# Kernel tuning notes

Hardware: AMD Instinct MI355X
Metric: run time of the kernel (lower is better)

## Reference

```python
import jax, jax.numpy as jnp
import numpy as np

N_DEG = 5
RANK = 4
SCALE = 4
IMW = IMH = 512
S = IMW * IMH
BATCH = 64
C_CH = 1


def setup_inputs() -> dict:
    key = jax.random.key(0)
    k1, k2, k3, k4 = jax.random.split(key, 4)
    x = jax.random.normal(k1, (BATCH, C_CH, IMW // SCALE, IMH // SCALE), dtype=jnp.float32)
    # CP-decomposed polynomial (CCP) factors; small init keeps degree-5 products stable
    A = jax.random.normal(k2, (N_DEG, RANK, S), dtype=jnp.float32) * 0.01
    C = jax.random.normal(k3, (S, RANK), dtype=jnp.float32) * 0.01
    b = jax.random.normal(k4, (S,), dtype=jnp.float32) * 0.01
    return {"x": x, "A": A, "C": C, "b": b}


def reference(x, A, C, b):
    bsize, c, w, h = x.shape
    # bilinear upsample, align_corners=False (half-pixel, matches torch default)
    up = jax.image.resize(x, (bsize, c, w * SCALE, h * SCALE), method="bilinear")
    flat = up.reshape(bsize, c, S)
    v = flat[:, c - 1, :]  # [B, S] -- original applies PolyLayer only to channel c-1
    # CCP polynomial network: z1 = A1 v; z_n = (A_n v) * z_{n-1} + z_{n-1}
    za = jnp.einsum("nrs,bs->bnr", A, v)  # [B, N, rank]
    z = za[:, 0]
    for n in range(1, N_DEG):
        z = za[:, n] * z + z
    out_v = jnp.einsum("br,sr->bs", z, C) + b  # [B, S]
    flat = flat.at[:, c - 1, :].set(out_v)
    return flat.reshape(bsize, c, w * SCALE, h * SCALE)
```

## Files before the change

### kernel.cpp

```cpp
#include <hip/hip_runtime.h>

#define S_TOTAL (512 * 512)
#define BATCH 64
#define KTOT2 16384

typedef float vfloat4 __attribute__((ext_vector_type(4)));
typedef float vfloat2 __attribute__((ext_vector_type(2)));

__device__ __forceinline__ float swz_x1(float v) {
    return __int_as_float(__builtin_amdgcn_ds_swizzle(__float_as_int(v), 0x041F));
}
__device__ __forceinline__ float swz_x2(float v) {
    return __int_as_float(__builtin_amdgcn_ds_swizzle(__float_as_int(v), 0x081F));
}
__device__ __forceinline__ float swz_x4(float v) {
    return __int_as_float(__builtin_amdgcn_ds_swizzle(__float_as_int(v), 0x101F));
}
__device__ __forceinline__ float swz_x8(float v) {
    return __int_as_float(__builtin_amdgcn_ds_swizzle(__float_as_int(v), 0x201F));
}

__global__ __launch_bounds__(256) void adjxy_kernel(
    const float* __restrict__ A,
    float* __restrict__ B2)
{
    __shared__ float arows[20][512];
    __shared__ float b1loc[20][128];

    const int t  = threadIdx.x;
    const int nr = blockIdx.x >> 5;
    const int tc = blockIdx.x & 31;
    const int y0 = 16 * tc - 2;

    const float* An = A + (size_t)nr * S_TOTAL;
#pragma unroll
    for (int i = t; i < 20 * 128; i += 256) {
        const int rl = i >> 7;
        const int q  = i & 127;
        const int y  = y0 + rl;
        vfloat4 v = {0.0f, 0.0f, 0.0f, 0.0f};
        if (y >= 0 && y < 512)
            v = *(const vfloat4*)(An + (size_t)y * 512 + q * 4);
        *(vfloat4*)&arows[rl][q * 4] = v;
    }
    __syncthreads();

#pragma unroll
    for (int i = t; i < 20 * 128; i += 256) {
        const int rl = i >> 7;
        const int j  = i & 127;
        const int base = 4 * j;
        const vfloat4 m0 = *(const vfloat4*)&arows[rl][max(base - 4, 0)];
        const vfloat4 m1 = *(const vfloat4*)&arows[rl][base];
        const vfloat4 m2 = *(const vfloat4*)&arows[rl][min(base + 4, 508)];
        float e0 = m0.z, e1 = m0.w, e6 = m2.x, e7 = m2.y;
        if (j == 0)   { e0 = 0.0f; e1 = 0.0f; }
        if (j == 127) { e6 = 0.0f; e7 = 0.0f; }
        float s = 0.125f * e0 + 0.375f * e1
                + 0.625f * m1.x + 0.875f * m1.y
                + 0.875f * m1.z + 0.625f * m1.w
                + 0.375f * e6 + 0.125f * e7;
        if (j == 0)   s += 0.375f * arows[rl][0]   + 0.125f * arows[rl][1];
        if (j == 127) s += 0.125f * arows[rl][510] + 0.375f * arows[rl][511];
        b1loc[rl][j] = s;
    }
    __syncthreads();

    const float w[8] = {0.125f, 0.375f, 0.625f, 0.875f,
                        0.875f, 0.625f, 0.375f, 0.125f};
#pragma unroll
    for (int i = t; i < 512; i += 256) {
        const int tyl = i >> 7;
        const int j   = i & 127;
        const int ty  = tc * 4 + tyl;
        float s = 0.0f;
#pragma unroll
        for (int p = 0; p < 8; ++p)
            s = fmaf(w[p], b1loc[4 * tyl + p][j], s);
        if (ty == 0)   s += 0.375f * b1loc[2][j]  + 0.125f * b1loc[3][j];
        if (ty == 127) s += 0.125f * b1loc[16][j] + 0.375f * b1loc[17][j];
        B2[(size_t)nr * KTOT2 + ty * 128 + j] = s;
    }
}

__global__ __launch_bounds__(512) void za_partial_kernel(
    const float* __restrict__ x,
    const float* __restrict__ B2,
    float* __restrict__ partial)
{
    const int t    = threadIdx.x;
    const int blk  = blockIdx.x;
    const int w    = t >> 6;
    const int lane = t & 63;
    const int b0   = w * 8;
    const size_t kbase = (size_t)blk * 256 + 4 * lane;

    vfloat4 xv[8];
#pragma unroll
    for (int bi = 0; bi < 8; ++bi)
        xv[bi] = *(const vfloat4*)(x + (size_t)(b0 + bi) * KTOT2 + kbase);

    float* pb = partial + (size_t)blk * 1280;
    const int lane1 = lane & 1, lane2 = lane & 2, lane4 = lane & 4, lane8 = lane & 8;

#pragma unroll
    for (int ch = 0; ch < 2; ++ch) {
        float acc[16][5];
#pragma unroll
        for (int v = 0; v < 16; ++v)
#pragma unroll
            for (int tt = 0; tt < 5; ++tt) acc[v][tt] = 0.0f;

#pragma unroll
        for (int tt = 0; tt < 5; ++tt)
#pragma unroll
            for (int par = 0; par < 2; ++par) {
                const int nr = ch * 10 + 2 * tt + par;
                const vfloat4 bq = *(const vfloat4*)(B2 + (size_t)nr * KTOT2 + kbase);
#pragma unroll
                for (int bi = 0; bi < 8; ++bi) {
                    acc[bi * 2 + par][tt] =
                        fmaf(bq.x, xv[bi].x, fmaf(bq.y, xv[bi].y,
                        fmaf(bq.z, xv[bi].z, fmaf(bq.w, xv[bi].w,
                             acc[bi * 2 + par][tt]))));
                }
            }

        float s1[8][5];
#pragma unroll
        for (int v = 0; v < 8; ++v)
#pragma unroll
            for (int tt = 0; tt < 5; ++tt) {
                const float u = acc[v][tt], h = acc[v + 8][tt];
                s1[v][tt] = (lane1 ? h : u) + swz_x1(lane1 ? u : h);
            }
        float s2[4][5];
#pragma unroll
        for (int v = 0; v < 4; ++v)
#pragma unroll
            for (int tt = 0; tt < 5; ++tt) {
                const float u = s1[v][tt], h = s1[v + 4][tt];
                s2[v][tt] = (lane2 ? h : u) + swz_x2(lane2 ? u : h);
            }
        float s3[2][5];
#pragma unroll
        for (int v = 0; v < 2; ++v)
#pragma unroll
            for (int tt = 0; tt < 5; ++tt) {
                const float u = s2[v][tt], h = s2[v + 2][tt];
                s3[v][tt] = (lane4 ? h : u) + swz_x4(lane4 ? u : h);
            }
        float s4[5];
#pragma unroll
        for (int tt = 0; tt < 5; ++tt) {
            const float u = s3[0][tt], h = s3[1][tt];
            s4[tt] = (lane8 ? h : u) + swz_x8(lane8 ? u : h);
        }
#pragma unroll
        for (int tt = 0; tt < 5; ++tt) {
            s4[tt] += __shfl_xor(s4[tt], 16, 64);
            s4[tt] += __shfl_xor(s4[tt], 32, 64);
        }

        if (lane < 16) {
            const int m = ((lane & 1) << 3) | ((lane & 2) << 1) |
                          ((lane & 4) >> 1) | ((lane & 8) >> 3);
            float* dst = pb + (b0 + (m >> 1)) * 20 + ch * 10 + (m & 1);
#pragma unroll
            for (int tt = 0; tt < 5; ++tt) dst[2 * tt] = s4[tt];
        }
    }
}

__global__ __launch_bounds__(256) void za_reduce_kernel(
    const float* __restrict__ partial, float* __restrict__ za)
{
    const int c = blockIdx.x * 256 + threadIdx.x;
    float a0 = 0, a1 = 0, a2 = 0, a3 = 0;
    for (int r = 0; r < 64; r += 4) {
        a0 += partial[(size_t)(r + 0) * 1280 + c];
        a1 += partial[(size_t)(r + 1) * 1280 + c];
        a2 += partial[(size_t)(r + 2) * 1280 + c];
        a3 += partial[(size_t)(r + 3) * 1280 + c];
    }
    za[c] = (a0 + a1) + (a2 + a3);
}

__global__ __launch_bounds__(256) void out_kernel(
    const float* __restrict__ C,
    const float* __restrict__ bias,
    const float* __restrict__ za,
    float* __restrict__ out)
{
    __shared__ float zs[BATCH][4];
    const int t = threadIdx.x;
    if (t < 64) {
#pragma unroll
        for (int r = 0; r < 4; ++r) {
            float zv = za[t * 20 + r];
#pragma unroll
            for (int n = 1; n < 5; ++n)
                zv *= (1.0f + za[t * 20 + n * 4 + r]);
            zs[t][r] = zv;
        }
    }
    __syncthreads();

    const int s0 = (blockIdx.x * 256 + t) * 2;
    const vfloat4 c0 = *(const vfloat4*)(C + (size_t)s0 * 4);
    const vfloat4 c1 = *(const vfloat4*)(C + (size_t)s0 * 4 + 4);
    const vfloat2 bv = *(const vfloat2*)(bias + s0);

#pragma unroll 8
    for (int bb = 0; bb < BATCH; ++bb) {
        const float z0 = zs[bb][0], z1 = zs[bb][1];
        const float z2 = zs[bb][2], z3 = zs[bb][3];
        vfloat2 o;
        o.x = fmaf(z0, c0.x, fmaf(z1, c0.y, fmaf(z2, c0.z, fmaf(z3, c0.w, bv.x))));
        o.y = fmaf(z0, c1.x, fmaf(z1, c1.y, fmaf(z2, c1.z, fmaf(z3, c1.w, bv.y))));
        __builtin_nontemporal_store(o, (vfloat2*)(out + (size_t)bb * S_TOTAL + s0));
    }
}

extern "C" void kernel_launch(void* const* d_in, const int* in_sizes, int n_in,
                              void* d_out, int out_size, void* d_ws, size_t ws_size,
                              hipStream_t stream)
{
    const float* x    = (const float*)d_in[0];
    const float* A    = (const float*)d_in[1];
    const float* C    = (const float*)d_in[2];
    const float* bias = (const float*)d_in[3];
    float* out = (float*)d_out;

    float* B2      = (float*)d_ws;
    float* partial = B2 + (size_t)20 * KTOT2;
    float* za      = partial + (size_t)64 * 1280;

    adjxy_kernel<<<640, 256, 0, stream>>>(A, B2);
    za_partial_kernel<<<64, 512, 0, stream>>>(x, B2, partial);
    za_reduce_kernel<<<5, 256, 0, stream>>>(partial, za);
    out_kernel<<<512, 256, 0, stream>>>(C, bias, za, out);
}
```

Baseline: 35.87 us.

## Fuse za reduction into partial kernel via last-block ticket and drop LDS staging

Removes the separate za_reduce kernel: each za_partial block increments an atomic counter, and the last block to finish sums all partials and computes the per-batch polynomial z values, writing them to a small global buffer. out_kernel now just loads the precomputed z values instead of recomputing them in every block. adjxy_kernel reads A directly from global memory rather than staging rows in shared memory first. A memset is added to reset the counter each call, and the final reduction runs serially in a single block.

```diff
diff --git a/kernel.cpp b/kernel.cpp
--- a/kernel.cpp
+++ b/kernel.cpp
@@ -3,6 +3,7 @@
 #define S_TOTAL (512 * 512)
 #define BATCH 64
 #define KTOT2 16384
+#define NBLK_ZA 64
 
 typedef float vfloat4 __attribute__((ext_vector_type(4)));
 typedef float vfloat2 __attribute__((ext_vector_type(2)));
@@ -24,7 +25,6 @@
     const float* __restrict__ A,
     float* __restrict__ B2)
 {
-    __shared__ float arows[20][512];
     __shared__ float b1loc[20][128];
 
     const int t  = threadIdx.x;
@@ -33,35 +33,29 @@
     const int y0 = 16 * tc - 2;
 
     const float* An = A + (size_t)nr * S_TOTAL;
-#pragma unroll
-    for (int i = t; i < 20 * 128; i += 256) {
-        const int rl = i >> 7;
-        const int q  = i & 127;
-        const int y  = y0 + rl;
-        vfloat4 v = {0.0f, 0.0f, 0.0f, 0.0f};
-        if (y >= 0 && y < 512)
-            v = *(const vfloat4*)(An + (size_t)y * 512 + q * 4);
-        *(vfloat4*)&arows[rl][q * 4] = v;
-    }
-    __syncthreads();
 
 #pragma unroll
     for (int i = t; i < 20 * 128; i += 256) {
         const int rl = i >> 7;
         const int j  = i & 127;
-        const int base = 4 * j;
-        const vfloat4 m0 = *(const vfloat4*)&arows[rl][max(base - 4, 0)];
-        const vfloat4 m1 = *(const vfloat4*)&arows[rl][base];
-        const vfloat4 m2 = *(const vfloat4*)&arows[rl][min(base + 4, 508)];
-        float e0 = m0.z, e1 = m0.w, e6 = m2.x, e7 = m2.y;
-        if (j == 0)   { e0 = 0.0f; e1 = 0.0f; }
-        if (j == 127) { e6 = 0.0f; e7 = 0.0f; }
-        float s = 0.125f * e0 + 0.375f * e1
-                + 0.625f * m1.x + 0.875f * m1.y
-                + 0.875f * m1.z + 0.625f * m1.w
-                + 0.375f * e6 + 0.125f * e7;
-        if (j == 0)   s += 0.375f * arows[rl][0]   + 0.125f * arows[rl][1];
-        if (j == 127) s += 0.125f * arows[rl][510] + 0.375f * arows[rl][511];
+        const int y  = y0 + rl;
+        float s = 0.0f;
+        if (y >= 0 && y < 512) {
+            const float* Ay = An + (size_t)y * 512;
+            const int base = 4 * j;
+            const vfloat4 m0 = *(const vfloat4*)(Ay + max(base - 4, 0));
+            const vfloat4 m1 = *(const vfloat4*)(Ay + base);
+            const vfloat4 m2 = *(const vfloat4*)(Ay + min(base + 4, 508));
+            float e0 = m0.z, e1 = m0.w, e6 = m2.x, e7 = m2.y;
+            if (j == 0)   { e0 = 0.0f; e1 = 0.0f; }
+            if (j == 127) { e6 = 0.0f; e7 = 0.0f; }
+            s = 0.125f * e0 + 0.375f * e1
+              + 0.625f * m1.x + 0.875f * m1.y
+              + 0.875f * m1.z + 0.625f * m1.w
+              + 0.375f * e6 + 0.125f * e7;
+            if (j == 0)   s += 0.375f * Ay[0]   + 0.125f * Ay[1];
+            if (j == 127) s += 0.125f * Ay[510] + 0.375f * Ay[511];
+        }
         b1loc[rl][j] = s;
     }
     __syncthreads();
@@ -86,8 +80,13 @@
 __global__ __launch_bounds__(512) void za_partial_kernel(
     const float* __restrict__ x,
     const float* __restrict__ B2,
-    float* __restrict__ partial)
-{
+    float* __restrict__ partial,
+    float* __restrict__ zg,
+    unsigned int* __restrict__ counter)
+{
+    __shared__ float za_lds[1280];
+    __shared__ unsigned int ticket;
+
     const int t    = threadIdx.x;
     const int blk  = blockIdx.x;
     const int w    = t >> 6;
@@ -170,40 +169,46 @@
             for (int tt = 0; tt < 5; ++tt) dst[2 * tt] = s4[tt];
         }
     }
-}
-
-__global__ __launch_bounds__(256) void za_reduce_kernel(
-    const float* __restrict__ partial, float* __restrict__ za)
-{
-    const int c = blockIdx.x * 256 + threadIdx.x;
-    float a0 = 0, a1 = 0, a2 = 0, a3 = 0;
-    for (int r = 0; r < 64; r += 4) {
-        a0 += partial[(size_t)(r + 0) * 1280 + c];
-        a1 += partial[(size_t)(r + 1) * 1280 + c];
-        a2 += partial[(size_t)(r + 2) * 1280 + c];
-        a3 += partial[(size_t)(r + 3) * 1280 + c];
-    }
-    za[c] = (a0 + a1) + (a2 + a3);
+
+    __threadfence();
+    __syncthreads();
+    if (t == 0) ticket = atomicAdd(counter, 1u);
+    __syncthreads();
+    if (ticket != NBLK_ZA - 1) return;
+
+    __threadfence();
+    for (int c = t; c < 1280; c += 512) {
+        float a0 = 0, a1 = 0, a2 = 0, a3 = 0;
+        for (int r = 0; r < NBLK_ZA; r += 4) {
+            a0 += partial[(size_t)(r + 0) * 1280 + c];
+            a1 += partial[(size_t)(r + 1) * 1280 + c];
+            a2 += partial[(size_t)(r + 2) * 1280 + c];
+            a3 += partial[(size_t)(r + 3) * 1280 + c];
+        }
+        za_lds[c] = (a0 + a1) + (a2 + a3);
+    }
+    __syncthreads();
+    if (t < 64) {
+#pragma unroll
+        for (int r = 0; r < 4; ++r) {
+            float zv = za_lds[t * 20 + r];
+#pragma unroll
+            for (int n = 1; n < 5; ++n)
+                zv *= (1.0f + za_lds[t * 20 + n * 4 + r]);
+            zg[t * 4 + r] = zv;
+        }
+    }
 }
 
 __global__ __launch_bounds__(256) void out_kernel(
     const float* __restrict__ C,
     const float* __restrict__ bias,
-    const float* __restrict__ za,
+    const float* __restrict__ zg,
     float* __restrict__ out)
 {
-    __shared__ float zs[BATCH][4];
+    __shared__ float zs[256];
     const int t = threadIdx.x;
-    if (t < 64) {
-#pragma unroll
-        for (int r = 0; r < 4; ++r) {
-            float zv = za[t * 20 + r];
-#pragma unroll
-            for (int n = 1; n < 5; ++n)
-                zv *= (1.0f + za[t * 20 + n * 4 + r]);
-            zs[t][r] = zv;
-        }
-    }
+    zs[t] = zg[t];
     __syncthreads();
 
     const int s0 = (blockIdx.x * 256 + t) * 2;
@@ -213,8 +218,8 @@
 
 #pragma unroll 8
     for (int bb = 0; bb < BATCH; ++bb) {
-        const float z0 = zs[bb][0], z1 = zs[bb][1];
-        const float z2 = zs[bb][2], z3 = zs[bb][3];
+        const float z0 = zs[bb * 4 + 0], z1 = zs[bb * 4 + 1];
+        const float z2 = zs[bb * 4 + 2], z3 = zs[bb * 4 + 3];
         vfloat2 o;
         o.x = fmaf(z0, c0.x, fmaf(z1, c0.y, fmaf(z2, c0.z, fmaf(z3, c0.w, bv.x))));
         o.y = fmaf(z0, c1.x, fmaf(z1, c1.y, fmaf(z2, c1.z, fmaf(z3, c1.w, bv.y))));
@@ -234,10 +239,11 @@
 
     float* B2      = (float*)d_ws;
     float* partial = B2 + (size_t)20 * KTOT2;
-    float* za      = partial + (size_t)64 * 1280;
-
+    float* zg      = partial + (size_t)NBLK_ZA * 1280;
+    unsigned int* counter = (unsigned int*)(zg + 256);
+
+    hipMemsetAsync(counter, 0, sizeof(unsigned int), stream);
     adjxy_kernel<<<640, 256, 0, stream>>>(A, B2);
-    za_partial_kernel<<<64, 512, 0, stream>>>(x, B2, partial);
-    za_reduce_kernel<<<5, 256, 0, stream>>>(partial, za);
-    out_kernel<<<512, 256, 0, stream>>>(C, bias, za, out);
-}
+    za_partial_kernel<<<NBLK_ZA, 512, 0, stream>>>(x, B2, partial, zg, counter);
+    out_kernel<<<512, 256, 0, stream>>>(C, bias, zg, out);
+}
```

Result: slower. 63.75 us (+77.7%).

## Spread za_partial over more blocks, widen out stores, drop adjxy LDS staging

Applied to the files above, without the earlier changes.

za_partial now launches four blocks per K chunk, each wave handling two batches instead of eight. This quadruples the grid and reduces register pressure and the length of the swizzle reduction. The out kernel writes float4 per thread and splits the batch range between two blocks, giving wider nontemporal stores. adjxy reads A directly from global memory instead of staging rows in LDS, which removes one barrier but issues redundant overlapping global loads.

```diff
diff --git a/kernel.cpp b/kernel.cpp
--- a/kernel.cpp
+++ b/kernel.cpp
@@ -3,9 +3,9 @@
 #define S_TOTAL (512 * 512)
 #define BATCH 64
 #define KTOT2 16384
+#define NKC 64
 
 typedef float vfloat4 __attribute__((ext_vector_type(4)));
-typedef float vfloat2 __attribute__((ext_vector_type(2)));
 
 __device__ __forceinline__ float swz_x1(float v) {
     return __int_as_float(__builtin_amdgcn_ds_swizzle(__float_as_int(v), 0x041F));
@@ -24,7 +24,6 @@
     const float* __restrict__ A,
     float* __restrict__ B2)
 {
-    __shared__ float arows[20][512];
     __shared__ float b1loc[20][128];
 
     const int t  = threadIdx.x;
@@ -33,35 +32,29 @@
     const int y0 = 16 * tc - 2;
 
     const float* An = A + (size_t)nr * S_TOTAL;
-#pragma unroll
-    for (int i = t; i < 20 * 128; i += 256) {
-        const int rl = i >> 7;
-        const int q  = i & 127;
-        const int y  = y0 + rl;
-        vfloat4 v = {0.0f, 0.0f, 0.0f, 0.0f};
-        if (y >= 0 && y < 512)
-            v = *(const vfloat4*)(An + (size_t)y * 512 + q * 4);
-        *(vfloat4*)&arows[rl][q * 4] = v;
-    }
-    __syncthreads();
 
 #pragma unroll
     for (int i = t; i < 20 * 128; i += 256) {
         const int rl = i >> 7;
         const int j  = i & 127;
-        const int base = 4 * j;
-        const vfloat4 m0 = *(const vfloat4*)&arows[rl][max(base - 4, 0)];
-        const vfloat4 m1 = *(const vfloat4*)&arows[rl][base];
-        const vfloat4 m2 = *(const vfloat4*)&arows[rl][min(base + 4, 508)];
-        float e0 = m0.z, e1 = m0.w, e6 = m2.x, e7 = m2.y;
-        if (j == 0)   { e0 = 0.0f; e1 = 0.0f; }
-        if (j == 127) { e6 = 0.0f; e7 = 0.0f; }
-        float s = 0.125f * e0 + 0.375f * e1
-                + 0.625f * m1.x + 0.875f * m1.y
-                + 0.875f * m1.z + 0.625f * m1.w
-                + 0.375f * e6 + 0.125f * e7;
-        if (j == 0)   s += 0.375f * arows[rl][0]   + 0.125f * arows[rl][1];
-        if (j == 127) s += 0.125f * arows[rl][510] + 0.375f * arows[rl][511];
+        const int y  = y0 + rl;
+        float s = 0.0f;
+        if (y >= 0 && y < 512) {
+            const float* Ay = An + (size_t)y * 512;
+            const int base = 4 * j;
+            const vfloat4 m0 = *(const vfloat4*)(Ay + max(base - 4, 0));
+            const vfloat4 m1 = *(const vfloat4*)(Ay + base);
+            const vfloat4 m2 = *(const vfloat4*)(Ay + min(base + 4, 508));
+            float e0 = m0.z, e1 = m0.w, e6 = m2.x, e7 = m2.y;
+            if (j == 0)   { e0 = 0.0f; e1 = 0.0f; }
+            if (j == 127) { e6 = 0.0f; e7 = 0.0f; }
+            s = 0.125f * e0 + 0.375f * e1
+              + 0.625f * m1.x + 0.875f * m1.y
+              + 0.875f * m1.z + 0.625f * m1.w
+              + 0.375f * e6 + 0.125f * e7;
+            if (j == 0)   s += 0.375f * Ay[0]   + 0.125f * Ay[1];
+            if (j == 127) s += 0.125f * Ay[510] + 0.375f * Ay[511];
+        }
         b1loc[rl][j] = s;
     }
     __syncthreads();
@@ -89,25 +82,24 @@
     float* __restrict__ partial)
 {
     const int t    = threadIdx.x;
-    const int blk  = blockIdx.x;
-    const int w    = t >> 6;
+    const int kc   = blockIdx.x >> 2;
+    const int bq   = blockIdx.x & 3;
+    const int wv   = t >> 6;
     const int lane = t & 63;
-    const int b0   = w * 8;
-    const size_t kbase = (size_t)blk * 256 + 4 * lane;
-
-    vfloat4 xv[8];
-#pragma unroll
-    for (int bi = 0; bi < 8; ++bi)
-        xv[bi] = *(const vfloat4*)(x + (size_t)(b0 + bi) * KTOT2 + kbase);
-
-    float* pb = partial + (size_t)blk * 1280;
-    const int lane1 = lane & 1, lane2 = lane & 2, lane4 = lane & 4, lane8 = lane & 8;
+    const int b0   = bq * 16 + wv * 2;
+    const size_t kbase = (size_t)kc * 256 + 4 * lane;
+
+    vfloat4 xv0 = *(const vfloat4*)(x + (size_t)b0 * KTOT2 + kbase);
+    vfloat4 xv1 = *(const vfloat4*)(x + (size_t)(b0 + 1) * KTOT2 + kbase);
+
+    float* pb = partial + (size_t)kc * 1280;
+    const int lane1 = lane & 1, lane2 = lane & 2;
 
 #pragma unroll
     for (int ch = 0; ch < 2; ++ch) {
-        float acc[16][5];
-#pragma unroll
-        for (int v = 0; v < 16; ++v)
+        float acc[4][5];
+#pragma unroll
+        for (int v = 0; v < 4; ++v)
 #pragma unroll
             for (int tt = 0; tt < 5; ++tt) acc[v][tt] = 0.0f;
 
@@ -116,58 +108,43 @@
 #pragma unroll
             for (int par = 0; par < 2; ++par) {
                 const int nr = ch * 10 + 2 * tt + par;
-                const vfloat4 bq = *(const vfloat4*)(B2 + (size_t)nr * KTOT2 + kbase);
-#pragma unroll
-                for (int bi = 0; bi < 8; ++bi) {
-                    acc[bi * 2 + par][tt] =
-                        fmaf(bq.x, xv[bi].x, fmaf(bq.y, xv[bi].y,
-                        fmaf(bq.z, xv[bi].z, fmaf(bq.w, xv[bi].w,
-                             acc[bi * 2 + par][tt]))));
-                }
+                const vfloat4 bq4 = *(const vfloat4*)(B2 + (size_t)nr * KTOT2 + kbase);
+                acc[par][tt] =
+                    fmaf(bq4.x, xv0.x, fmaf(bq4.y, xv0.y,
+                    fmaf(bq4.z, xv0.z, fmaf(bq4.w, xv0.w, acc[par][tt]))));
+                acc[2 + par][tt] =
+                    fmaf(bq4.x, xv1.x, fmaf(bq4.y, xv1.y,
+                    fmaf(bq4.z, xv1.z, fmaf(bq4.w, xv1.w, acc[2 + par][tt]))));
             }
 
-        float s1[8][5];
-#pragma unroll
-        for (int v = 0; v < 8; ++v)
+        float s1[2][5];
+#pragma unroll
+        for (int v = 0; v < 2; ++v)
 #pragma unroll
             for (int tt = 0; tt < 5; ++tt) {
-                const float u = acc[v][tt], h = acc[v + 8][tt];
+                const float u = acc[v][tt], h = acc[v + 2][tt];
                 s1[v][tt] = (lane1 ? h : u) + swz_x1(lane1 ? u : h);
             }
-        float s2[4][5];
-#pragma unroll
-        for (int v = 0; v < 4; ++v)
-#pragma unroll
-            for (int tt = 0; tt < 5; ++tt) {
-                const float u = s1[v][tt], h = s1[v + 4][tt];
-                s2[v][tt] = (lane2 ? h : u) + swz_x2(lane2 ? u : h);
-            }
-        float s3[2][5];
-#pragma unroll
-        for (int v = 0; v < 2; ++v)
-#pragma unroll
-            for (int tt = 0; tt < 5; ++tt) {
-                const float u = s2[v][tt], h = s2[v + 2][tt];
-                s3[v][tt] = (lane4 ? h : u) + swz_x4(lane4 ? u : h);
-            }
-        float s4[5];
+        float s2[5];
 #pragma unroll
         for (int tt = 0; tt < 5; ++tt) {
-            const float u = s3[0][tt], h = s3[1][tt];
-            s4[tt] = (lane8 ? h : u) + swz_x8(lane8 ? u : h);
+            const float u = s1[0][tt], h = s1[1][tt];
+            s2[tt] = (lane2 ? h : u) + swz_x2(lane2 ? u : h);
         }
 #pragma unroll
         for (int tt = 0; tt < 5; ++tt) {
-            s4[tt] += __shfl_xor(s4[tt], 16, 64);
-            s4[tt] += __shfl_xor(s4[tt], 32, 64);
-        }
-
-        if (lane < 16) {
-            const int m = ((lane & 1) << 3) | ((lane & 2) << 1) |
-                          ((lane & 4) >> 1) | ((lane & 8) >> 3);
-            float* dst = pb + (b0 + (m >> 1)) * 20 + ch * 10 + (m & 1);
-#pragma unroll
-            for (int tt = 0; tt < 5; ++tt) dst[2 * tt] = s4[tt];
+            s2[tt] += swz_x4(s2[tt]);
+            s2[tt] += swz_x8(s2[tt]);
+            s2[tt] += __shfl_xor(s2[tt], 16, 64);
+            s2[tt] += __shfl_xor(s2[tt], 32, 64);
+        }
+
+        if (lane < 4) {
+            const int bi  = lane & 1;
+            const int par = (lane >> 1) & 1;
+            float* dst = pb + (size_t)(b0 + bi) * 20 + ch * 10 + par;
+#pragma unroll
+            for (int tt = 0; tt < 5; ++tt) dst[2 * tt] = s2[tt];
         }
     }
 }
@@ -177,7 +154,7 @@
 {
     const int c = blockIdx.x * 256 + threadIdx.x;
     float a0 = 0, a1 = 0, a2 = 0, a3 = 0;
-    for (int r = 0; r < 64; r += 4) {
+    for (int r = 0; r < NKC; r += 4) {
         a0 += partial[(size_t)(r + 0) * 1280 + c];
         a1 += partial[(size_t)(r + 1) * 1280 + c];
         a2 += partial[(size_t)(r + 2) * 1280 + c];
@@ -192,7 +169,7 @@
     const float* __restrict__ za,
     float* __restrict__ out)
 {
-    __shared__ float zs[BATCH][4];
+    __shared__ float zs[256];
     const int t = threadIdx.x;
     if (t < 64) {
 #pragma unroll
@@ -201,24 +178,30 @@
 #pragma unroll
             for (int n = 1; n < 5; ++n)
                 zv *= (1.0f + za[t * 20 + n * 4 + r]);
-            zs[t][r] = zv;
+            zs[t * 4 + r] = zv;
         }
     }
     __syncthreads();
 
-    const int s0 = (blockIdx.x * 256 + t) * 2;
+    const int sb = blockIdx.x >> 1;
+    const int bh = blockIdx.x & 1;
+    const int s0 = (sb * 256 + t) * 4;
     const vfloat4 c0 = *(const vfloat4*)(C + (size_t)s0 * 4);
     const vfloat4 c1 = *(const vfloat4*)(C + (size_t)s0 * 4 + 4);
-    const vfloat2 bv = *(const vfloat2*)(bias + s0);
+    const vfloat4 c2 = *(const vfloat4*)(C + (size_t)s0 * 4 + 8);
+    const vfloat4 c3 = *(const vfloat4*)(C + (size_t)s0 * 4 + 12);
+    const vfloat4 bv = *(const vfloat4*)(bias + s0);
 
 #pragma unroll 8
-    for (int bb = 0; bb < BATCH; ++bb) {
-        const float z0 = zs[bb][0], z1 = zs[bb][1];
-        const float z2 = zs[bb][2], z3 = zs[bb][3];
-        vfloat2 o;
+    for (int bb = bh * 32; bb < bh * 32 + 32; ++bb) {
+        const float z0 = zs[bb * 4 + 0], z1 = zs[bb * 4 + 1];
+        const float z2 = zs[bb * 4 + 2], z3 = zs[bb * 4 + 3];
+        vfloat4 o;
         o.x = fmaf(z0, c0.x, fmaf(z1, c0.y, fmaf(z2, c0.z, fmaf(z3, c0.w, bv.x))));
         o.y = fmaf(z0, c1.x, fmaf(z1, c1.y, fmaf(z2, c1.z, fmaf(z3, c1.w, bv.y))));
-        __builtin_nontemporal_store(o, (vfloat2*)(out + (size_t)bb * S_TOTAL + s0));
+        o.z = fmaf(z0, c2.x, fmaf(z1, c2.y, fmaf(z2, c2.z, fmaf(z3, c2.w, bv.z))));
+        o.w = fmaf(z0, c3.x, fmaf(z1, c3.y, fmaf(z2, c3.z, fmaf(z3, c3.w, bv.w))));
+        __builtin_nontemporal_store(o, (vfloat4*)(out + (size_t)bb * S_TOTAL + s0));
     }
 }
 
@@ -234,10 +217,10 @@
 
     float* B2      = (float*)d_ws;
     float* partial = B2 + (size_t)20 * KTOT2;
-    float* za      = partial + (size_t)64 * 1280;
+    float* za      = partial + (size_t)NKC * 1280;
 
     adjxy_kernel<<<640, 256, 0, stream>>>(A, B2);
-    za_partial_kernel<<<64, 512, 0, stream>>>(x, B2, partial);
+    za_partial_kernel<<<256, 512, 0, stream>>>(x, B2, partial);
     za_reduce_kernel<<<5, 256, 0, stream>>>(partial, za);
     out_kernel<<<512, 256, 0, stream>>>(C, bias, za, out);
 }
```

New measurement: 34.93 us. 1.03x faster.
